# Kernel optimization log

Measured on AMD Instinct MI355X. Metric: run time of the kernel, lower is better.

Reference implementation:

```python
import jax, jax.numpy as jnp
import numpy as np

TEMPERATURE = 8.0  # sqrt(dim_k=64)
NEG_INF = -1e30    # stand-in for -inf that stays finite-safe under softmax


def setup_inputs() -> dict:
    key = jax.random.key(0)
    kq, kk, kv, km = jax.random.split(key, 4)
    bsz, lq, lk, d = 64, 2048, 2048, 64
    q = jax.random.normal(kq, (bsz, lq, d), dtype=jnp.float32)
    k = jax.random.normal(kk, (bsz, lk, d), dtype=jnp.float32)
    v = jax.random.normal(kv, (bsz, lk, d), dtype=jnp.float32)
    mask = jax.random.normal(km, (bsz, lq, lk), dtype=jnp.float32)
    return {"q": q, "k": k, "v": v, "mask": mask}


def reference(q, k, v, mask):
    # attn = QK^T / temperature, additive graph mask, threshold -inf fill
    attn = jnp.einsum("bqd,bkd->bqk", q, k) / TEMPERATURE
    attn = attn + mask                       # graph_mask_type == 'add'
    attn = jnp.where(mask < 0, NEG_INF, attn)  # masked_fill(mask.lt(0), -inf)
    attn = jax.nn.softmax(attn, axis=2)
    # dropout p=0.0 -> identity
    output = jnp.einsum("bqk,bkd->bqd", attn, v)
    return (output, attn)
```

## Files before the change

### kernel.cpp

```cpp
#include <hip/hip_runtime.h>
#include <stdint.h>
#include <stddef.h>


typedef __attribute__((ext_vector_type(4))) float f32x4;
typedef __fp16 f16x2 __attribute__((ext_vector_type(2)));
typedef __fp16 f16x4 __attribute__((ext_vector_type(4)));
typedef __fp16 f16x8 __attribute__((ext_vector_type(8)));

static constexpr int BATCH = 64;
static constexpr int SEQ   = 2048;
static constexpr int HD    = 64;
static constexpr float NEGH = -60000.0f;

__global__ void kfrag_kernel(const float* __restrict__ k, __fp16* __restrict__ kf) {
  const int b    = blockIdx.x >> 5;
  const int ch   = blockIdx.x & 31;
  const int tid  = threadIdx.x;
  const int tl   = tid >> 6;
  const int lane = tid & 63;
  const int l15  = lane & 15;
  const int g    = lane >> 4;
  const int kt   = ch * 4 + tl;
  const float* src = k + ((size_t)(b * SEQ + kt * 16 + l15)) * HD + g * 8;
  char* dst = (char*)kf + ((size_t)(b * 128 + kt)) * 2048 + l15 * 64 + g * 16;
#pragma unroll
  for (int half = 0; half < 2; ++half) {
    f32x4 a = *(const f32x4*)(src + half * 32);
    f32x4 c = *(const f32x4*)(src + half * 32 + 4);
    f16x2 p0 = __builtin_amdgcn_cvt_pkrtz(a[0], a[1]);
    f16x2 p1 = __builtin_amdgcn_cvt_pkrtz(a[2], a[3]);
    f16x2 p2 = __builtin_amdgcn_cvt_pkrtz(c[0], c[1]);
    f16x2 p3 = __builtin_amdgcn_cvt_pkrtz(c[2], c[3]);
    f16x8 o;
    o[0] = p0[0]; o[1] = p0[1]; o[2] = p1[0]; o[3] = p1[1];
    o[4] = p2[0]; o[5] = p2[1]; o[6] = p3[0]; o[7] = p3[1];
    *(f16x8*)(dst + half * 1024) = o;
  }
}

__global__ void vfrag_kernel(const float* __restrict__ v, __fp16* __restrict__ vf) {
  __shared__ float tile[64][68];
  const int b   = blockIdx.x >> 5;
  const int ch  = blockIdx.x & 31;
  const int tid = threadIdx.x;
  const int kk  = tid >> 4;
  const int d4  = (tid & 15) << 2;
  const int k0  = ch * 64;
#pragma unroll
  for (int i = 0; i < 4; ++i) {
    f32x4 val = *(const f32x4*)(v + ((size_t)(b * SEQ + k0 + kk + 16 * i)) * HD + d4);
    tile[kk + 16 * i][d4 + 0] = val[0];
    tile[kk + 16 * i][d4 + 1] = val[1];
    tile[kk + 16 * i][d4 + 2] = val[2];
    tile[kk + 16 * i][d4 + 3] = val[3];
  }
  __syncthreads();
  const int tl  = tid >> 6;
  const int db  = (tid >> 4) & 3;
  const int l15 = tid & 15;
  f16x8 o0, o1;
#pragma unroll
  for (int g = 0; g < 2; ++g)
#pragma unroll
    for (int j = 0; j < 4; ++j)
      o0[g * 4 + j] = (__fp16)tile[tl * 16 + g * 4 + j][db * 16 + l15];
#pragma unroll
  for (int g = 0; g < 2; ++g)
#pragma unroll
    for (int j = 0; j < 4; ++j)
      o1[g * 4 + j] = (__fp16)tile[tl * 16 + (g + 2) * 4 + j][db * 16 + l15];
  char* dst = (char*)vf + ((size_t)(b * 128 + ch * 4 + tl)) * 2048 + db * 512 + l15 * 32;
  *(f16x8*)(dst)      = o0;
  *(f16x8*)(dst + 16) = o1;
}

__global__ __launch_bounds__(256, 2) void attn_kernel(
    const float* __restrict__ q,
    const __fp16* __restrict__ kf,
    const __fp16* __restrict__ vf,
    const float* __restrict__ mask,
    float* __restrict__ out,
    float* __restrict__ attn) {
  __shared__ __align__(16) char pool[4][4352];
  __shared__ float stat_m[4][16];
  __shared__ float stat_l[4][16];

  const int tid  = threadIdx.x;
  const int w    = tid >> 6;
  const int lane = tid & 63;
  const int l15  = lane & 15;
  const int g    = lane >> 4;
  const int g4   = g << 2;

  const int bid = blockIdx.x;
  const int xcd = bid & 7;
  const int r   = bid >> 3;
  const int b   = xcd * 8 + (r >> 7);
  const int q0  = (r & 127) << 4;
  const int wk0 = w << 9;

  char* wb = pool[w];
  const int koff = l15 * 64 + g * 16;
  const int voff = l15 * 32 + g * 8;

  const char* kfb = (const char*)kf + ((size_t)(b * 128) + w * 32) * 2048;
  const char* vfb = (const char*)vf + ((size_t)(b * 128) + w * 32) * 2048;
  const float* mbase = mask + ((size_t)(b * SEQ + q0)) * SEQ + wk0;
  float*       abase = attn + ((size_t)(b * SEQ + q0)) * SEQ + wk0;

  f16x8 qb0, qb1;
  {
    const float* qsrc = q + ((size_t)(b * SEQ + q0 + l15)) * HD + g * 8;
    f32x4 a0 = *(const f32x4*)(qsrc);
    f32x4 a1 = *(const f32x4*)(qsrc + 4);
    f32x4 c0 = *(const f32x4*)(qsrc + 32);
    f32x4 c1 = *(const f32x4*)(qsrc + 36);
    f16x2 p0 = __builtin_amdgcn_cvt_pkrtz(a0[0], a0[1]);
    f16x2 p1 = __builtin_amdgcn_cvt_pkrtz(a0[2], a0[3]);
    f16x2 p2 = __builtin_amdgcn_cvt_pkrtz(a1[0], a1[1]);
    f16x2 p3 = __builtin_amdgcn_cvt_pkrtz(a1[2], a1[3]);
    qb0[0] = p0[0]; qb0[1] = p0[1]; qb0[2] = p1[0]; qb0[3] = p1[1];
    qb0[4] = p2[0]; qb0[5] = p2[1]; qb0[6] = p3[0]; qb0[7] = p3[1];
    p0 = __builtin_amdgcn_cvt_pkrtz(c0[0], c0[1]);
    p1 = __builtin_amdgcn_cvt_pkrtz(c0[2], c0[3]);
    p2 = __builtin_amdgcn_cvt_pkrtz(c1[0], c1[1]);
    p3 = __builtin_amdgcn_cvt_pkrtz(c1[2], c1[3]);
    qb1[0] = p0[0]; qb1[1] = p0[1]; qb1[2] = p1[0]; qb1[3] = p1[1];
    qb1[4] = p2[0]; qb1[5] = p2[1]; qb1[6] = p3[0]; qb1[7] = p3[1];
  }

  f16x4 PH0,  PH1,  PH2,  PH3,  PH4,  PH5,  PH6,  PH7;
  f16x4 PH8,  PH9,  PH10, PH11, PH12, PH13, PH14, PH15;
  f16x4 PH16, PH17, PH18, PH19, PH20, PH21, PH22, PH23;
  f16x4 PH24, PH25, PH26, PH27, PH28, PH29, PH30, PH31;

  f16x8 K0A, K0B, K1A, K1B, K2A, K2B, K3A, K3B;
  f16x8 K4A, K4B, K5A, K5B, K6A, K6B, K7A, K7B;
  f32x4 MA0, MA1, MA2, MA3;
  f32x4 MB0, MB1, MB2, MB3;
  float m = -3.0e38f;

#define ISSUE_K(t, KA, KB)                                                   \
  KA = *(const f16x8*)(kfb + (size_t)(t) * 2048 + koff);                     \
  KB = *(const f16x8*)(kfb + (size_t)(t) * 2048 + 1024 + koff);

#define ISSUE_M(c, M0, M1, M2, M3)                                           \
  M0 = __builtin_nontemporal_load((const f32x4*)(mbase + (size_t)(0 * 4 + g) * SEQ + (c) * 64 + l15 * 4)); \
  M1 = __builtin_nontemporal_load((const f32x4*)(mbase + (size_t)(1 * 4 + g) * SEQ + (c) * 64 + l15 * 4)); \
  M2 = __builtin_nontemporal_load((const f32x4*)(mbase + (size_t)(2 * 4 + g) * SEQ + (c) * 64 + l15 * 4)); \
  M3 = __builtin_nontemporal_load((const f32x4*)(mbase + (size_t)(3 * 4 + g) * SEQ + (c) * 64 + l15 * 4));

#define WRITE_M(M0, M1, M2, M3)                                              \
  *(f32x4*)(wb + (0 * 4 + g) * 272 + l15 * 16) = M0;                         \
  *(f32x4*)(wb + (1 * 4 + g) * 272 + l15 * 16) = M1;                         \
  *(f32x4*)(wb + (2 * 4 + g) * 272 + l15 * 16) = M2;                         \
  *(f32x4*)(wb + (3 * 4 + g) * 272 + l15 * 16) = M3;

#define ATILE(t, PH, KA, KB)                                                 \
  {                                                                          \
    f32x4 acc = {0.f, 0.f, 0.f, 0.f};                                        \
    acc = __builtin_amdgcn_mfma_f32_16x16x32_f16(KA, qb0, acc, 0, 0, 0);     \
    acc = __builtin_amdgcn_mfma_f32_16x16x32_f16(KB, qb1, acc, 0, 0, 0);     \
    const f32x4 mv = *(const f32x4*)(wb + l15 * 272 + ((t) & 3) * 64 + g * 16); \
    float s0 = (mv[0] < 0.f) ? NEGH : fmaf(acc[0], 0.125f, mv[0]);           \
    float s1 = (mv[1] < 0.f) ? NEGH : fmaf(acc[1], 0.125f, mv[1]);           \
    float s2 = (mv[2] < 0.f) ? NEGH : fmaf(acc[2], 0.125f, mv[2]);           \
    float s3 = (mv[3] < 0.f) ? NEGH : fmaf(acc[3], 0.125f, mv[3]);           \
    m = fmaxf(m, fmaxf(fmaxf(s0, s1), fmaxf(s2, s3)));                       \
    f16x2 lo_ = __builtin_amdgcn_cvt_pkrtz(s0, s1);                          \
    f16x2 hi_ = __builtin_amdgcn_cvt_pkrtz(s2, s3);                          \
    PH = (f16x4){lo_[0], lo_[1], hi_[0], hi_[1]};                            \
  }

#define AT(t, PH, KA, KB)  ATILE(t, PH, KA, KB) ISSUE_K((t) + 8, KA, KB)
#define ATL(t, PH, KA, KB) ATILE(t, PH, KA, KB)

  ISSUE_M(0, MA0, MA1, MA2, MA3)
  ISSUE_K(0, K0A, K0B) ISSUE_K(1, K1A, K1B) ISSUE_K(2, K2A, K2B) ISSUE_K(3, K3A, K3B)
  ISSUE_M(1, MB0, MB1, MB2, MB3)
  ISSUE_K(4, K4A, K4B) ISSUE_K(5, K5A, K5B) ISSUE_K(6, K6A, K6B) ISSUE_K(7, K7A, K7B)

  WRITE_M(MA0, MA1, MA2, MA3) ISSUE_M(2, MA0, MA1, MA2, MA3)
  AT(0, PH0, K0A, K0B)  AT(1, PH1, K1A, K1B)  AT(2, PH2, K2A, K2B)  AT(3, PH3, K3A, K3B)
  WRITE_M(MB0, MB1, MB2, MB3) ISSUE_M(3, MB0, MB1, MB2, MB3)
  AT(4, PH4, K4A, K4B)  AT(5, PH5, K5A, K5B)  AT(6, PH6, K6A, K6B)  AT(7, PH7, K7A, K7B)
  WRITE_M(MA0, MA1, MA2, MA3) ISSUE_M(4, MA0, MA1, MA2, MA3)
  AT(8, PH8, K0A, K0B)  AT(9, PH9, K1A, K1B)  AT(10, PH10, K2A, K2B) AT(11, PH11, K3A, K3B)
  WRITE_M(MB0, MB1, MB2, MB3) ISSUE_M(5, MB0, MB1, MB2, MB3)
  AT(12, PH12, K4A, K4B) AT(13, PH13, K5A, K5B) AT(14, PH14, K6A, K6B) AT(15, PH15, K7A, K7B)
  WRITE_M(MA0, MA1, MA2, MA3) ISSUE_M(6, MA0, MA1, MA2, MA3)
  AT(16, PH16, K0A, K0B) AT(17, PH17, K1A, K1B) AT(18, PH18, K2A, K2B) AT(19, PH19, K3A, K3B)
  WRITE_M(MB0, MB1, MB2, MB3) ISSUE_M(7, MB0, MB1, MB2, MB3)
  AT(20, PH20, K4A, K4B) AT(21, PH21, K5A, K5B) AT(22, PH22, K6A, K6B) AT(23, PH23, K7A, K7B)
  WRITE_M(MA0, MA1, MA2, MA3)
  ATL(24, PH24, K0A, K0B) ATL(25, PH25, K1A, K1B) ATL(26, PH26, K2A, K2B) ATL(27, PH27, K3A, K3B)
  WRITE_M(MB0, MB1, MB2, MB3)
  ATL(28, PH28, K4A, K4B) ATL(29, PH29, K5A, K5B) ATL(30, PH30, K6A, K6B) ATL(31, PH31, K7A, K7B)

#undef AT
#undef ATL
#undef ATILE
#undef ISSUE_K
#undef ISSUE_M
#undef WRITE_M

  m = fmaxf(m, __shfl_xor(m, 16));
  m = fmaxf(m, __shfl_xor(m, 32));

  float lw = 0.f;
#define A2_STEP(PH)                                                          \
  {                                                                          \
    float e0 = __expf((float)PH[0] - m);                                     \
    float e1 = __expf((float)PH[1] - m);                                     \
    float e2 = __expf((float)PH[2] - m);                                     \
    float e3 = __expf((float)PH[3] - m);                                     \
    lw += (e0 + e1) + (e2 + e3);                                             \
    f16x2 lo_ = __builtin_amdgcn_cvt_pkrtz(e0, e1);                          \
    f16x2 hi_ = __builtin_amdgcn_cvt_pkrtz(e2, e3);                          \
    PH = (f16x4){lo_[0], lo_[1], hi_[0], hi_[1]};                            \
  }
  A2_STEP(PH0)  A2_STEP(PH1)  A2_STEP(PH2)  A2_STEP(PH3)
  A2_STEP(PH4)  A2_STEP(PH5)  A2_STEP(PH6)  A2_STEP(PH7)
  A2_STEP(PH8)  A2_STEP(PH9)  A2_STEP(PH10) A2_STEP(PH11)
  A2_STEP(PH12) A2_STEP(PH13) A2_STEP(PH14) A2_STEP(PH15)
  A2_STEP(PH16) A2_STEP(PH17) A2_STEP(PH18) A2_STEP(PH19)
  A2_STEP(PH20) A2_STEP(PH21) A2_STEP(PH22) A2_STEP(PH23)
  A2_STEP(PH24) A2_STEP(PH25) A2_STEP(PH26) A2_STEP(PH27)
  A2_STEP(PH28) A2_STEP(PH29) A2_STEP(PH30) A2_STEP(PH31)
#undef A2_STEP

  lw += __shfl_xor(lw, 16);
  lw += __shfl_xor(lw, 32);

  if (lane < 16) { stat_m[w][lane] = m; stat_l[w][lane] = lw; }
  __syncthreads();

  float mg = -3.0e38f;
#pragma unroll
  for (int ww = 0; ww < 4; ++ww) mg = fmaxf(mg, stat_m[ww][l15]);
  float lg = 0.f;
#pragma unroll
  for (int ww = 0; ww < 4; ++ww) lg += stat_l[ww][l15] * __expf(stat_m[ww][l15] - mg);
  const float scale = __expf(m - mg) / lg;
  const __fp16 hs = (__fp16)scale;
  const f16x4 sc4 = {hs, hs, hs, hs};

  f32x4 oacc0 = {0.f, 0.f, 0.f, 0.f};
  f32x4 oacc1 = {0.f, 0.f, 0.f, 0.f};
  f32x4 oacc2 = {0.f, 0.f, 0.f, 0.f};
  f32x4 oacc3 = {0.f, 0.f, 0.f, 0.f};

  f16x4 V0a, V0b, V0c, V0d, V1a, V1b, V1c, V1d;
  f16x4 V2a, V2b, V2c, V2d, V3a, V3b, V3c, V3d;

#define ISSUE_V(t, Va, Vb, Vc, Vd)                                           \
  Va = *(const f16x4*)(vfb + (size_t)(t) * 2048 + 0 * 512 + voff);           \
  Vb = *(const f16x4*)(vfb + (size_t)(t) * 2048 + 1 * 512 + voff);           \
  Vc = *(const f16x4*)(vfb + (size_t)(t) * 2048 + 2 * 512 + voff);           \
  Vd = *(const f16x4*)(vfb + (size_t)(t) * 2048 + 3 * 512 + voff);

#define BTILE(t, PH, Va, Vb, Vc, Vd)                                         \
  {                                                                          \
    const f16x4 pf = PH * sc4;                                               \
    f32x4 st;                                                                \
    st[0] = (float)pf[0]; st[1] = (float)pf[1];                              \
    st[2] = (float)pf[2]; st[3] = (float)pf[3];                              \
    *(f32x4*)(wb + l15 * 272 + ((t) & 3) * 64 + g * 16) = st;                \
    oacc0 = __builtin_amdgcn_mfma_f32_16x16x16f16(Va, pf, oacc0, 0, 0, 0);   \
    oacc1 = __builtin_amdgcn_mfma_f32_16x16x16f16(Vb, pf, oacc1, 0, 0, 0);   \
    oacc2 = __builtin_amdgcn_mfma_f32_16x16x16f16(Vc, pf, oacc2, 0, 0, 0);   \
    oacc3 = __builtin_amdgcn_mfma_f32_16x16x16f16(Vd, pf, oacc3, 0, 0, 0);   \
  }

#define STORE_A(c)                                                           \
  __builtin_nontemporal_store(                                               \
      *(const f32x4*)(wb + (0 * 4 + g) * 272 + l15 * 16),                    \
      (f32x4*)(abase + (size_t)(0 * 4 + g) * SEQ + (c) * 64 + l15 * 4));     \
  __builtin_nontemporal_store(                                               \
      *(const f32x4*)(wb + (1 * 4 + g) * 272 + l15 * 16),                    \
      (f32x4*)(abase + (size_t)(1 * 4 + g) * SEQ + (c) * 64 + l15 * 4));     \
  __builtin_nontemporal_store(                                               \
      *(const f32x4*)(wb + (2 * 4 + g) * 272 + l15 * 16),                    \
      (f32x4*)(abase + (size_t)(2 * 4 + g) * SEQ + (c) * 64 + l15 * 4));     \
  __builtin_nontemporal_store(                                               \
      *(const f32x4*)(wb + (3 * 4 + g) * 272 + l15 * 16),                    \
      (f32x4*)(abase + (size_t)(3 * 4 + g) * SEQ + (c) * 64 + l15 * 4));

#define BS(t, PH, Va, Vb, Vc, Vd)  BTILE(t, PH, Va, Vb, Vc, Vd) ISSUE_V((t) + 4, Va, Vb, Vc, Vd)
#define BSL(t, PH, Va, Vb, Vc, Vd) BTILE(t, PH, Va, Vb, Vc, Vd)

  ISSUE_V(0, V0a, V0b, V0c, V0d) ISSUE_V(1, V1a, V1b, V1c, V1d)
  ISSUE_V(2, V2a, V2b, V2c, V2d) ISSUE_V(3, V3a, V3b, V3c, V3d)

  BS(0, PH0, V0a, V0b, V0c, V0d)   BS(1, PH1, V1a, V1b, V1c, V1d)
  BS(2, PH2, V2a, V2b, V2c, V2d)   BS(3, PH3, V3a, V3b, V3c, V3d)   STORE_A(0)
  BS(4, PH4, V0a, V0b, V0c, V0d)   BS(5, PH5, V1a, V1b, V1c, V1d)
  BS(6, PH6, V2a, V2b, V2c, V2d)   BS(7, PH7, V3a, V3b, V3c, V3d)   STORE_A(1)
  BS(8, PH8, V0a, V0b, V0c, V0d)   BS(9, PH9, V1a, V1b, V1c, V1d)
  BS(10, PH10, V2a, V2b, V2c, V2d) BS(11, PH11, V3a, V3b, V3c, V3d) STORE_A(2)
  BS(12, PH12, V0a, V0b, V0c, V0d) BS(13, PH13, V1a, V1b, V1c, V1d)
  BS(14, PH14, V2a, V2b, V2c, V2d) BS(15, PH15, V3a, V3b, V3c, V3d) STORE_A(3)
  BS(16, PH16, V0a, V0b, V0c, V0d) BS(17, PH17, V1a, V1b, V1c, V1d)
  BS(18, PH18, V2a, V2b, V2c, V2d) BS(19, PH19, V3a, V3b, V3c, V3d) STORE_A(4)
  BS(20, PH20, V0a, V0b, V0c, V0d) BS(21, PH21, V1a, V1b, V1c, V1d)
  BS(22, PH22, V2a, V2b, V2c, V2d) BS(23, PH23, V3a, V3b, V3c, V3d) STORE_A(5)
  BS(24, PH24, V0a, V0b, V0c, V0d) BS(25, PH25, V1a, V1b, V1c, V1d)
  BS(26, PH26, V2a, V2b, V2c, V2d) BS(27, PH27, V3a, V3b, V3c, V3d) STORE_A(6)
  BSL(28, PH28, V0a, V0b, V0c, V0d) BSL(29, PH29, V1a, V1b, V1c, V1d)
  BSL(30, PH30, V2a, V2b, V2c, V2d) BSL(31, PH31, V3a, V3b, V3c, V3d) STORE_A(7)

#undef BS
#undef BSL
#undef BTILE
#undef ISSUE_V
#undef STORE_A

  float* sred_w = (float*)pool[w];
#pragma unroll
  for (int rr = 0; rr < 4; ++rr) {
    sred_w[(0 * 16 + g4 + rr) * 17 + l15] = oacc0[rr];
    sred_w[(1 * 16 + g4 + rr) * 17 + l15] = oacc1[rr];
    sred_w[(2 * 16 + g4 + rr) * 17 + l15] = oacc2[rr];
    sred_w[(3 * 16 + g4 + rr) * 17 + l15] = oacc3[rr];
  }
  __syncthreads();

#pragma unroll
  for (int ii = 0; ii < 4; ++ii) {
    const int i = tid + ii * 256;
    const int qq = i >> 6;
    const int d = i & 63;
    const int o = d * 17 + qq;
    float s = ((const float*)pool[0])[o] + ((const float*)pool[1])[o] +
              ((const float*)pool[2])[o] + ((const float*)pool[3])[o];
    out[((size_t)(b * SEQ + q0 + qq)) * HD + d] = s;
  }
}

extern "C" void kernel_launch(void* const* d_in, const int* in_sizes, int n_in,
                              void* d_out, int out_size, void* d_ws, size_t ws_size,
                              hipStream_t stream) {
  const float* q    = (const float*)d_in[0];
  const float* k    = (const float*)d_in[1];
  const float* v    = (const float*)d_in[2];
  const float* mask = (const float*)d_in[3];

  float* out  = (float*)d_out;
  float* attn = out + (size_t)BATCH * SEQ * HD;

  const size_t nqk = (size_t)BATCH * SEQ * HD;
  __fp16* kfrag = (__fp16*)d_ws;
  __fp16* vfrag = kfrag + nqk;

  kfrag_kernel<<<dim3(BATCH * 32), dim3(256), 0, stream>>>(k, kfrag);
  vfrag_kernel<<<dim3(BATCH * 32), dim3(256), 0, stream>>>(v, vfrag);
  attn_kernel<<<dim3(BATCH * (SEQ / 16)), dim3(256), 0, stream>>>(q, kfrag, vfrag, mask, out, attn);
}
```

Baseline: 540.0 us.

## Merge fragment kernels, online softmax stats, shallower K prefetch, occupancy 3

Folds the K and V fragment-conversion kernels into one launch. In the attention kernel, the K prefetch depth drops from 8 tiles to 4, freeing registers so launch bounds can move from 2 to 3 waves per SIMD. It also replaces the separate exponentiation pass with an online running max and sum computed during score tiles. The final exponentials are now recomputed in fp32 during the PV stage and written directly, which adds more exp work per element in exchange for fewer live registers and a pass removed. The shallower prefetch may expose more memory latency.

```diff
diff --git a/kernel.cpp b/kernel.cpp
--- a/kernel.cpp
+++ b/kernel.cpp
@@ -13,69 +13,71 @@
 static constexpr int HD    = 64;
 static constexpr float NEGH = -60000.0f;
 
-__global__ void kfrag_kernel(const float* __restrict__ k, __fp16* __restrict__ kf) {
-  const int b    = blockIdx.x >> 5;
-  const int ch   = blockIdx.x & 31;
-  const int tid  = threadIdx.x;
-  const int tl   = tid >> 6;
-  const int lane = tid & 63;
-  const int l15  = lane & 15;
-  const int g    = lane >> 4;
-  const int kt   = ch * 4 + tl;
-  const float* src = k + ((size_t)(b * SEQ + kt * 16 + l15)) * HD + g * 8;
-  char* dst = (char*)kf + ((size_t)(b * 128 + kt)) * 2048 + l15 * 64 + g * 16;
-#pragma unroll
-  for (int half = 0; half < 2; ++half) {
-    f32x4 a = *(const f32x4*)(src + half * 32);
-    f32x4 c = *(const f32x4*)(src + half * 32 + 4);
-    f16x2 p0 = __builtin_amdgcn_cvt_pkrtz(a[0], a[1]);
-    f16x2 p1 = __builtin_amdgcn_cvt_pkrtz(a[2], a[3]);
-    f16x2 p2 = __builtin_amdgcn_cvt_pkrtz(c[0], c[1]);
-    f16x2 p3 = __builtin_amdgcn_cvt_pkrtz(c[2], c[3]);
-    f16x8 o;
-    o[0] = p0[0]; o[1] = p0[1]; o[2] = p1[0]; o[3] = p1[1];
-    o[4] = p2[0]; o[5] = p2[1]; o[6] = p3[0]; o[7] = p3[1];
-    *(f16x8*)(dst + half * 1024) = o;
+__global__ void frag_kernel(const float* __restrict__ k, const float* __restrict__ v,
+                            __fp16* __restrict__ kf, __fp16* __restrict__ vf) {
+  __shared__ float tile[64][68];
+  if (blockIdx.x < 2048) {
+    const int b    = blockIdx.x >> 5;
+    const int ch   = blockIdx.x & 31;
+    const int tid  = threadIdx.x;
+    const int tl   = tid >> 6;
+    const int lane = tid & 63;
+    const int l15  = lane & 15;
+    const int g    = lane >> 4;
+    const int kt   = ch * 4 + tl;
+    const float* src = k + ((size_t)(b * SEQ + kt * 16 + l15)) * HD + g * 8;
+    char* dst = (char*)kf + ((size_t)(b * 128 + kt)) * 2048 + l15 * 64 + g * 16;
+#pragma unroll
+    for (int half = 0; half < 2; ++half) {
+      f32x4 a = *(const f32x4*)(src + half * 32);
+      f32x4 c = *(const f32x4*)(src + half * 32 + 4);
+      f16x2 p0 = __builtin_amdgcn_cvt_pkrtz(a[0], a[1]);
+      f16x2 p1 = __builtin_amdgcn_cvt_pkrtz(a[2], a[3]);
+      f16x2 p2 = __builtin_amdgcn_cvt_pkrtz(c[0], c[1]);
+      f16x2 p3 = __builtin_amdgcn_cvt_pkrtz(c[2], c[3]);
+      f16x8 o;
+      o[0] = p0[0]; o[1] = p0[1]; o[2] = p1[0]; o[3] = p1[1];
+      o[4] = p2[0]; o[5] = p2[1]; o[6] = p3[0]; o[7] = p3[1];
+      *(f16x8*)(dst + half * 1024) = o;
+    }
+  } else {
+    const int bid = blockIdx.x - 2048;
+    const int b   = bid >> 5;
+    const int ch  = bid & 31;
+    const int tid = threadIdx.x;
+    const int kk  = tid >> 4;
+    const int d4  = (tid & 15) << 2;
+    const int k0  = ch * 64;
+#pragma unroll
+    for (int i = 0; i < 4; ++i) {
+      f32x4 val = *(const f32x4*)(v + ((size_t)(b * SEQ + k0 + kk + 16 * i)) * HD + d4);
+      tile[kk + 16 * i][d4 + 0] = val[0];
+      tile[kk + 16 * i][d4 + 1] = val[1];
+      tile[kk + 16 * i][d4 + 2] = val[2];
+      tile[kk + 16 * i][d4 + 3] = val[3];
+    }
+    __syncthreads();
+    const int tl  = tid >> 6;
+    const int db  = (tid >> 4) & 3;
+    const int l15 = tid & 15;
+    f16x8 o0, o1;
+#pragma unroll
+    for (int g = 0; g < 2; ++g)
+#pragma unroll
+      for (int j = 0; j < 4; ++j)
+        o0[g * 4 + j] = (__fp16)tile[tl * 16 + g * 4 + j][db * 16 + l15];
+#pragma unroll
+    for (int g = 0; g < 2; ++g)
+#pragma unroll
+      for (int j = 0; j < 4; ++j)
+        o1[g * 4 + j] = (__fp16)tile[tl * 16 + (g + 2) * 4 + j][db * 16 + l15];
+    char* dst = (char*)vf + ((size_t)(b * 128 + ch * 4 + tl)) * 2048 + db * 512 + l15 * 32;
+    *(f16x8*)(dst)      = o0;
+    *(f16x8*)(dst + 16) = o1;
   }
 }
 
-__global__ void vfrag_kernel(const float* __restrict__ v, __fp16* __restrict__ vf) {
-  __shared__ float tile[64][68];
-  const int b   = blockIdx.x >> 5;
-  const int ch  = blockIdx.x & 31;
-  const int tid = threadIdx.x;
-  const int kk  = tid >> 4;
-  const int d4  = (tid & 15) << 2;
-  const int k0  = ch * 64;
-#pragma unroll
-  for (int i = 0; i < 4; ++i) {
-    f32x4 val = *(const f32x4*)(v + ((size_t)(b * SEQ + k0 + kk + 16 * i)) * HD + d4);
-    tile[kk + 16 * i][d4 + 0] = val[0];
-    tile[kk + 16 * i][d4 + 1] = val[1];
-    tile[kk + 16 * i][d4 + 2] = val[2];
-    tile[kk + 16 * i][d4 + 3] = val[3];
-  }
-  __syncthreads();
-  const int tl  = tid >> 6;
-  const int db  = (tid >> 4) & 3;
-  const int l15 = tid & 15;
-  f16x8 o0, o1;
-#pragma unroll
-  for (int g = 0; g < 2; ++g)
-#pragma unroll
-    for (int j = 0; j < 4; ++j)
-      o0[g * 4 + j] = (__fp16)tile[tl * 16 + g * 4 + j][db * 16 + l15];
-#pragma unroll
-  for (int g = 0; g < 2; ++g)
-#pragma unroll
-    for (int j = 0; j < 4; ++j)
-      o1[g * 4 + j] = (__fp16)tile[tl * 16 + (g + 2) * 4 + j][db * 16 + l15];
-  char* dst = (char*)vf + ((size_t)(b * 128 + ch * 4 + tl)) * 2048 + db * 512 + l15 * 32;
-  *(f16x8*)(dst)      = o0;
-  *(f16x8*)(dst + 16) = o1;
-}
-
-__global__ __launch_bounds__(256, 2) void attn_kernel(
+__global__ __launch_bounds__(256, 3) void attn_kernel(
     const float* __restrict__ q,
     const __fp16* __restrict__ kf,
     const __fp16* __restrict__ vf,
@@ -136,10 +138,10 @@
   f16x4 PH24, PH25, PH26, PH27, PH28, PH29, PH30, PH31;
 
   f16x8 K0A, K0B, K1A, K1B, K2A, K2B, K3A, K3B;
-  f16x8 K4A, K4B, K5A, K5B, K6A, K6B, K7A, K7B;
   f32x4 MA0, MA1, MA2, MA3;
   f32x4 MB0, MB1, MB2, MB3;
   float m = -3.0e38f;
+  float l = 0.f;
 
 #define ISSUE_K(t, KA, KB)                                                   \
   KA = *(const f16x8*)(kfb + (size_t)(t) * 2048 + koff);                     \
@@ -167,36 +169,39 @@
     float s1 = (mv[1] < 0.f) ? NEGH : fmaf(acc[1], 0.125f, mv[1]);           \
     float s2 = (mv[2] < 0.f) ? NEGH : fmaf(acc[2], 0.125f, mv[2]);           \
     float s3 = (mv[3] < 0.f) ? NEGH : fmaf(acc[3], 0.125f, mv[3]);           \
-    m = fmaxf(m, fmaxf(fmaxf(s0, s1), fmaxf(s2, s3)));                       \
+    const float tm = fmaxf(fmaxf(s0, s1), fmaxf(s2, s3));                    \
+    const float nm = fmaxf(m, tm);                                           \
+    l = l * __expf(m - nm) + __expf(s0 - nm) + __expf(s1 - nm)               \
+        + __expf(s2 - nm) + __expf(s3 - nm);                                 \
+    m = nm;                                                                  \
     f16x2 lo_ = __builtin_amdgcn_cvt_pkrtz(s0, s1);                          \
     f16x2 hi_ = __builtin_amdgcn_cvt_pkrtz(s2, s3);                          \
     PH = (f16x4){lo_[0], lo_[1], hi_[0], hi_[1]};                            \
   }
 
-#define AT(t, PH, KA, KB)  ATILE(t, PH, KA, KB) ISSUE_K((t) + 8, KA, KB)
+#define AT(t, PH, KA, KB)  ATILE(t, PH, KA, KB) ISSUE_K((t) + 4, KA, KB)
 #define ATL(t, PH, KA, KB) ATILE(t, PH, KA, KB)
 
   ISSUE_M(0, MA0, MA1, MA2, MA3)
   ISSUE_K(0, K0A, K0B) ISSUE_K(1, K1A, K1B) ISSUE_K(2, K2A, K2B) ISSUE_K(3, K3A, K3B)
   ISSUE_M(1, MB0, MB1, MB2, MB3)
-  ISSUE_K(4, K4A, K4B) ISSUE_K(5, K5A, K5B) ISSUE_K(6, K6A, K6B) ISSUE_K(7, K7A, K7B)
 
   WRITE_M(MA0, MA1, MA2, MA3) ISSUE_M(2, MA0, MA1, MA2, MA3)
   AT(0, PH0, K0A, K0B)  AT(1, PH1, K1A, K1B)  AT(2, PH2, K2A, K2B)  AT(3, PH3, K3A, K3B)
   WRITE_M(MB0, MB1, MB2, MB3) ISSUE_M(3, MB0, MB1, MB2, MB3)
-  AT(4, PH4, K4A, K4B)  AT(5, PH5, K5A, K5B)  AT(6, PH6, K6A, K6B)  AT(7, PH7, K7A, K7B)
+  AT(4, PH4, K0A, K0B)  AT(5, PH5, K1A, K1B)  AT(6, PH6, K2A, K2B)  AT(7, PH7, K3A, K3B)
   WRITE_M(MA0, MA1, MA2, MA3) ISSUE_M(4, MA0, MA1, MA2, MA3)
   AT(8, PH8, K0A, K0B)  AT(9, PH9, K1A, K1B)  AT(10, PH10, K2A, K2B) AT(11, PH11, K3A, K3B)
   WRITE_M(MB0, MB1, MB2, MB3) ISSUE_M(5, MB0, MB1, MB2, MB3)
-  AT(12, PH12, K4A, K4B) AT(13, PH13, K5A, K5B) AT(14, PH14, K6A, K6B) AT(15, PH15, K7A, K7B)
+  AT(12, PH12, K0A, K0B) AT(13, PH13, K1A, K1B) AT(14, PH14, K2A, K2B) AT(15, PH15, K3A, K3B)
   WRITE_M(MA0, MA1, MA2, MA3) ISSUE_M(6, MA0, MA1, MA2, MA3)
   AT(16, PH16, K0A, K0B) AT(17, PH17, K1A, K1B) AT(18, PH18, K2A, K2B) AT(19, PH19, K3A, K3B)
   WRITE_M(MB0, MB1, MB2, MB3) ISSUE_M(7, MB0, MB1, MB2, MB3)
-  AT(20, PH20, K4A, K4B) AT(21, PH21, K5A, K5B) AT(22, PH22, K6A, K6B) AT(23, PH23, K7A, K7B)
+  AT(20, PH20, K0A, K0B) AT(21, PH21, K1A, K1B) AT(22, PH22, K2A, K2B) AT(23, PH23, K3A, K3B)
   WRITE_M(MA0, MA1, MA2, MA3)
-  ATL(24, PH24, K0A, K0B) ATL(25, PH25, K1A, K1B) ATL(26, PH26, K2A, K2B) ATL(27, PH27, K3A, K3B)
+  AT(24, PH24, K0A, K0B) AT(25, PH25, K1A, K1B) AT(26, PH26, K2A, K2B) AT(27, PH27, K3A, K3B)
   WRITE_M(MB0, MB1, MB2, MB3)
-  ATL(28, PH28, K4A, K4B) ATL(29, PH29, K5A, K5B) ATL(30, PH30, K6A, K6B) ATL(31, PH31, K7A, K7B)
+  ATL(28, PH28, K0A, K0B) ATL(29, PH29, K1A, K1B) ATL(30, PH30, K2A, K2B) ATL(31, PH31, K3A, K3B)
 
 #undef AT
 #undef ATL
@@ -205,35 +210,14 @@
 #undef ISSUE_M
 #undef WRITE_M
 
-  m = fmaxf(m, __shfl_xor(m, 16));
-  m = fmaxf(m, __shfl_xor(m, 32));
-
-  float lw = 0.f;
-#define A2_STEP(PH)                                                          \
-  {                                                                          \
-    float e0 = __expf((float)PH[0] - m);                                     \
-    float e1 = __expf((float)PH[1] - m);                                     \
-    float e2 = __expf((float)PH[2] - m);                                     \
-    float e3 = __expf((float)PH[3] - m);                                     \
-    lw += (e0 + e1) + (e2 + e3);                                             \
-    f16x2 lo_ = __builtin_amdgcn_cvt_pkrtz(e0, e1);                          \
-    f16x2 hi_ = __builtin_amdgcn_cvt_pkrtz(e2, e3);                          \
-    PH = (f16x4){lo_[0], lo_[1], hi_[0], hi_[1]};                            \
-  }
-  A2_STEP(PH0)  A2_STEP(PH1)  A2_STEP(PH2)  A2_STEP(PH3)
-  A2_STEP(PH4)  A2_STEP(PH5)  A2_STEP(PH6)  A2_STEP(PH7)
-  A2_STEP(PH8)  A2_STEP(PH9)  A2_STEP(PH10) A2_STEP(PH11)
-  A2_STEP(PH12) A2_STEP(PH13) A2_STEP(PH14) A2_STEP(PH15)
-  A2_STEP(PH16) A2_STEP(PH17) A2_STEP(PH18) A2_STEP(PH19)
-  A2_STEP(PH20) A2_STEP(PH21) A2_STEP(PH22) A2_STEP(PH23)
-  A2_STEP(PH24) A2_STEP(PH25) A2_STEP(PH26) A2_STEP(PH27)
-  A2_STEP(PH28) A2_STEP(PH29) A2_STEP(PH30) A2_STEP(PH31)
-#undef A2_STEP
-
-  lw += __shfl_xor(lw, 16);
-  lw += __shfl_xor(lw, 32);
-
-  if (lane < 16) { stat_m[w][lane] = m; stat_l[w][lane] = lw; }
+  {
+    float mw = fmaxf(m, __shfl_xor(m, 16));
+    mw = fmaxf(mw, __shfl_xor(mw, 32));
+    float lad = l * __expf(m - mw);
+    lad += __shfl_xor(lad, 16);
+    lad += __shfl_xor(lad, 32);
+    if (lane < 16) { stat_m[w][lane] = mw; stat_l[w][lane] = lad; }
+  }
   __syncthreads();
 
   float mg = -3.0e38f;
@@ -242,9 +226,7 @@
   float lg = 0.f;
 #pragma unroll
   for (int ww = 0; ww < 4; ++ww) lg += stat_l[ww][l15] * __expf(stat_m[ww][l15] - mg);
-  const float scale = __expf(m - mg) / lg;
-  const __fp16 hs = (__fp16)scale;
-  const f16x4 sc4 = {hs, hs, hs, hs};
+  const float rl = 1.0f / lg;
 
   f32x4 oacc0 = {0.f, 0.f, 0.f, 0.f};
   f32x4 oacc1 = {0.f, 0.f, 0.f, 0.f};
@@ -262,11 +244,16 @@
 
 #define BTILE(t, PH, Va, Vb, Vc, Vd)                                         \
   {                                                                          \
-    const f16x4 pf = PH * sc4;                                               \
+    float e0 = __expf((float)PH[0] - mg) * rl;                               \
+    float e1 = __expf((float)PH[1] - mg) * rl;                               \
+    float e2 = __expf((float)PH[2] - mg) * rl;                               \
+    float e3 = __expf((float)PH[3] - mg) * rl;                               \
     f32x4 st;                                                                \
-    st[0] = (float)pf[0]; st[1] = (float)pf[1];                              \
-    st[2] = (float)pf[2]; st[3] = (float)pf[3];                              \
+    st[0] = e0; st[1] = e1; st[2] = e2; st[3] = e3;                          \
     *(f32x4*)(wb + l15 * 272 + ((t) & 3) * 64 + g * 16) = st;                \
+    f16x2 lo_ = __builtin_amdgcn_cvt_pkrtz(e0, e1);                          \
+    f16x2 hi_ = __builtin_amdgcn_cvt_pkrtz(e2, e3);                          \
+    const f16x4 pf = (f16x4){lo_[0], lo_[1], hi_[0], hi_[1]};                \
     oacc0 = __builtin_amdgcn_mfma_f32_16x16x16f16(Va, pf, oacc0, 0, 0, 0);   \
     oacc1 = __builtin_amdgcn_mfma_f32_16x16x16f16(Vb, pf, oacc1, 0, 0, 0);   \
     oacc2 = __builtin_amdgcn_mfma_f32_16x16x16f16(Vc, pf, oacc2, 0, 0, 0);   \
@@ -353,7 +340,6 @@
   __fp16* kfrag = (__fp16*)d_ws;
   __fp16* vfrag = kfrag + nqk;
 
-  kfrag_kernel<<<dim3(BATCH * 32), dim3(256), 0, stream>>>(k, kfrag);
-  vfrag_kernel<<<dim3(BATCH * 32), dim3(256), 0, stream>>>(v, vfrag);
+  frag_kernel<<<dim3(2 * BATCH * 32), dim3(256), 0, stream>>>(k, v, kfrag, vfrag);
   attn_kernel<<<dim3(BATCH * (SEQ / 16)), dim3(256), 0, stream>>>(q, kfrag, vfrag, mask, out, attn);
 }
```

Result: slower. 589.9 us (+9.2%).
